# Kernel optimization log

Measured on AMD Instinct MI355X. Metric: run time of the kernel, lower is better.

Reference implementation:

```python
import jax, jax.numpy as jnp
import numpy as np
from jax import lax

B, H, W = 16, 1024, 1024


def _bayer_masks(h, w, pattern='RGGB'):
    ch = {c: np.zeros((h, w), dtype=bool) for c in 'RGB'}
    for c, (y, x) in zip(pattern.upper(), [(0, 0), (0, 1), (1, 0), (1, 1)]):
        ch[c][y::2, x::2] = True
    return ch['R'], ch['G'], ch['B']


def _kernels():
    GR_GB = np.asarray([[0, 0, -1, 0, 0], [0, 0, 2, 0, 0], [-1, 2, 4, 2, -1],
                        [0, 0, 2, 0, 0], [0, 0, -1, 0, 0]], dtype=np.float64) / 8
    Rg_RB_Bg_BR = np.asarray([[0, 0, 0.5, 0, 0], [0, -1, 0, -1, 0], [-1, 4, 5, 4, -1],
                              [0, -1, 0, -1, 0], [0, 0, 0.5, 0, 0]], dtype=np.float64) / 8
    Rg_BR_Bg_RB = Rg_RB_Bg_BR.T
    Rb_BB_Br_RR = np.asarray([[0, 0, -1.5, 0, 0], [0, 2, 0, 2, 0], [-1.5, 0, 6, 0, -1.5],
                              [0, 2, 0, 2, 0], [0, 0, -1.5, 0, 0]], dtype=np.float64) / 8
    # torch code stores rot90(k=2) copies and feeds them to F.conv2d (cross-correlation)
    rot = lambda k: np.ascontiguousarray(np.rot90(k, 2)).astype(np.float32)
    return rot(GR_GB), rot(Rg_RB_Bg_BR), rot(Rg_BR_Bg_RB), rot(Rb_BB_Br_RR)


def setup_inputs() -> dict:
    key = jax.random.key(0)
    cfa = jax.random.uniform(key, (B, 1, H, W), dtype=jnp.float32)
    k1, k2, k3, k4 = _kernels()
    return {
        'CFA_inputs': cfa,
        'GR_GB': jnp.asarray(k1),
        'Rg_RB_Bg_BR': jnp.asarray(k2),
        'Rg_BR_Bg_RB': jnp.asarray(k3),
        'Rb_BB_Br_RR': jnp.asarray(k4),
    }


def _conv5(x, k):  # x: [B,1,H,W], k: [5,5]; cross-correlation, padding=2
    return lax.conv_general_dilated(
        x, k[None, None].astype(x.dtype), (1, 1), ((2, 2), (2, 2)),
        dimension_numbers=('NCHW', 'OIHW', 'NCHW'))


def reference(CFA_inputs, GR_GB, Rg_RB_Bg_BR, Rg_BR_Bg_RB, Rb_BB_Br_RR):
    h, w = CFA_inputs.shape[2], CFA_inputs.shape[3]
    R_m, G_m, B_m = _bayer_masks(h, w, 'RGGB')

    # static row/column selector masks (numpy, concrete at trace time)
    R_r = np.any(R_m, axis=1)[:, None] & np.ones((h, w), dtype=bool)
    R_c = np.any(R_m, axis=0)[None, :] & np.ones((h, w), dtype=bool)
    B_r = np.any(B_m, axis=1)[:, None] & np.ones((h, w), dtype=bool)
    B_c = np.any(B_m, axis=0)[None, :] & np.ones((h, w), dtype=bool)

    m = lambda a: jnp.asarray(a[None, None])  # -> [1,1,H,W] bool

    R = CFA_inputs * m(R_m).astype(CFA_inputs.dtype)
    G = CFA_inputs * m(G_m).astype(CFA_inputs.dtype)
    Bp = CFA_inputs * m(B_m).astype(CFA_inputs.dtype)

    GR_GB_res = _conv5(CFA_inputs, GR_GB)
    RBg_RBBR = _conv5(CFA_inputs, Rg_RB_Bg_BR)
    RBg_BRRB = _conv5(CFA_inputs, Rg_BR_Bg_RB)
    RBgr_BBRR = _conv5(CFA_inputs, Rb_BB_Br_RR)

    G = jnp.where(m(R_m | B_m), GR_GB_res, G)

    Rr_Bc = m(R_r & B_c)
    Br_Rc = m(B_r & R_c)
    Br_Bc = m(B_r & B_c)
    Rr_Rc = m(R_r & R_c)

    R = jnp.where(Rr_Bc, RBg_RBBR, R)
    R = jnp.where(Br_Rc, RBg_BRRB, R)
    Bp = jnp.where(Br_Rc, RBg_RBBR, Bp)
    Bp = jnp.where(Rr_Bc, RBg_BRRB, Bp)
    R = jnp.where(Br_Bc, RBgr_BBRR, R)
    Bp = jnp.where(Rr_Rc, RBgr_BBRR, Bp)

    return jnp.concatenate([R, G, Bp], axis=1)  # [B,3,H,W]
```

## Files before the change

### kernel.cpp

```cpp
#include <hip/hip_runtime.h>


constexpr int Bn = 16, Hn = 1024, Wn = 1024;
constexpr int RS = 16;

typedef float vfloat4 __attribute__((ext_vector_type(4)));

__global__ __launch_bounds__(256) void demosaic_v3(
    const float* __restrict__ src, float* __restrict__ out)
{
    const int t  = threadIdx.x;
    const int y0 = blockIdx.x * RS;
    const int b  = blockIdx.y;

    const float* sb = sb = src + (size_t)b * Hn * Wn;

    const bool tL = (t == 0);
    const bool tR = (t == 255);
    const int xl = tL ? 0 : (4 * t - 4);
    const int xr = tR ? (Wn - 4) : (4 * t + 4);

    float row[5][8];

    auto loadrow = [&](int gy, float* r) {
        const bool valid = ((unsigned)gy < (unsigned)Hn);
        const int gyc = valid ? gy : 0;
        const float* p = sb + (size_t)gyc * Wn;
        const vfloat4 c  = *(const vfloat4*)(p + 4 * t);
        const vfloat4 lq = *(const vfloat4*)(p + xl);
        const vfloat4 rq = *(const vfloat4*)(p + xr);
        r[0] = tL ? 0.f : lq.z;
        r[1] = tL ? 0.f : lq.w;
        r[2] = c.x; r[3] = c.y; r[4] = c.z; r[5] = c.w;
        r[6] = tR ? 0.f : rq.x;
        r[7] = tR ? 0.f : rq.y;
        if (!valid) {
            #pragma unroll
            for (int k = 0; k < 8; ++k) r[k] = 0.f;
        }
    };

    #pragma unroll
    for (int i = 0; i < 4; ++i) loadrow(y0 - 2 + i, row[i]);

    const size_t HW = (size_t)Hn * Wn;
    float* ob = out + (size_t)b * 3 * HW + (size_t)y0 * Wn + 4 * t;

    #pragma unroll
    for (int i = 0; i < RS; ++i) {
        loadrow(y0 + i + 2, row[(i + 4) % 5]);

        const float* r0 = row[(i + 0) % 5];
        const float* r1 = row[(i + 1) % 5];
        const float* r2 = row[(i + 2) % 5];
        const float* r3 = row[(i + 3) % 5];
        const float* r4 = row[(i + 4) % 5];

        float R[4], G[4], Bc[4];
        #pragma unroll
        for (int j = 0; j < 4; ++j) {
            const float c   = r2[j + 2];
            const float h1  = r2[j + 1] + r2[j + 3];
            const float v1  = r1[j + 2] + r3[j + 2];
            const float h2  = r2[j] + r2[j + 4];
            const float v2s = r0[j + 2] + r4[j + 2];
            const float ax2 = h2 + v2s;
            const float dg  = r1[j + 1] + r1[j + 3] + r3[j + 1] + r3[j + 3];

            const int py = i & 1;
            const int px = j & 1;
            if (px == 0 && py == 0) {
                R[j] = c;
                G[j] = 0.5f * c + 0.25f * (h1 + v1) - 0.125f * ax2;
                Bc[j] = 0.75f * c + 0.25f * dg - 0.1875f * ax2;
            } else if (px == 1 && py == 0) {
                R[j] = 0.625f * c + 0.5f * h1 - 0.125f * h2 + 0.0625f * v2s - 0.125f * dg;
                G[j] = c;
                Bc[j] = 0.625f * c + 0.5f * v1 - 0.125f * v2s + 0.0625f * h2 - 0.125f * dg;
            } else if (px == 0 && py == 1) {
                R[j] = 0.625f * c + 0.5f * v1 - 0.125f * v2s + 0.0625f * h2 - 0.125f * dg;
                G[j] = c;
                Bc[j] = 0.625f * c + 0.5f * h1 - 0.125f * h2 + 0.0625f * v2s - 0.125f * dg;
            } else {
                R[j] = 0.75f * c + 0.25f * dg - 0.1875f * ax2;
                G[j] = 0.5f * c + 0.25f * (h1 + v1) - 0.125f * ax2;
                Bc[j] = c;
            }
        }

        vfloat4 r4v = {R[0], R[1], R[2], R[3]};
        vfloat4 g4v = {G[0], G[1], G[2], G[3]};
        vfloat4 b4v = {Bc[0], Bc[1], Bc[2], Bc[3]};
        float* o = ob + (size_t)i * Wn;
        __builtin_nontemporal_store(r4v, (vfloat4*)o);
        __builtin_nontemporal_store(g4v, (vfloat4*)(o + HW));
        __builtin_nontemporal_store(b4v, (vfloat4*)(o + 2 * HW));
    }
}

extern "C" void kernel_launch(void* const* d_in, const int* in_sizes, int n_in,
                              void* d_out, int out_size, void* d_ws, size_t ws_size,
                              hipStream_t stream) {
    const float* cfa = (const float*)d_in[0];
    float* out = (float*)d_out;

    dim3 grid(Hn / RS, Bn);
    demosaic_v3<<<grid, dim3(256), 0, stream>>>(cfa, out);
}
```

Measured before the change: 259.4 us.

## Use 4-row tiles with all halo rows loaded upfront instead of rolling window

Each block now handles 4 output rows instead of 16 and loads all 8 needed input rows (center plus left/right quads) at the start rather than streaming one row per iteration. This raises memory-level parallelism and quadruples the number of blocks. The cost is more redundant halo reads, about 2x input re-reading instead of 1.25x, and more registers per thread.

Result: no change. 254.6 us (-1.9%).

```diff
diff --git a/kernel.cpp b/kernel.cpp
--- a/kernel.cpp
+++ b/kernel.cpp
@@ -2,59 +2,61 @@
 
 
 constexpr int Bn = 16, Hn = 1024, Wn = 1024;
-constexpr int RS = 16;
+constexpr int TR = 4;
 
 typedef float vfloat4 __attribute__((ext_vector_type(4)));
 
-__global__ __launch_bounds__(256) void demosaic_v3(
+__global__ __launch_bounds__(256) void demosaic_v4(
     const float* __restrict__ src, float* __restrict__ out)
 {
     const int t  = threadIdx.x;
-    const int y0 = blockIdx.x * RS;
+    const int y0 = blockIdx.x * TR;
     const int b  = blockIdx.y;
 
-    const float* sb = sb = src + (size_t)b * Hn * Wn;
+    const float* sb = src + (size_t)b * Hn * Wn;
 
     const bool tL = (t == 0);
     const bool tR = (t == 255);
-    const int xl = tL ? 0 : (4 * t - 4);
-    const int xr = tR ? (Wn - 4) : (4 * t + 4);
+    const int xc = 4 * t;
+    const int xl = tL ? 0 : xc - 4;
+    const int xr = tR ? (Wn - 4) : (xc + 4);
 
-    float row[5][8];
+    vfloat4 Lq[8], Cq[8], Rq[8];
+    #pragma unroll
+    for (int r = 0; r < 8; ++r) {
+        int gy = y0 - 2 + r;
+        int gyc = gy < 0 ? 0 : (gy > Hn - 1 ? Hn - 1 : gy);
+        const float* p = sb + (size_t)gyc * Wn;
+        Cq[r] = *(const vfloat4*)(p + xc);
+        Lq[r] = *(const vfloat4*)(p + xl);
+        Rq[r] = *(const vfloat4*)(p + xr);
+    }
 
-    auto loadrow = [&](int gy, float* r) {
-        const bool valid = ((unsigned)gy < (unsigned)Hn);
-        const int gyc = valid ? gy : 0;
-        const float* p = sb + (size_t)gyc * Wn;
-        const vfloat4 c  = *(const vfloat4*)(p + 4 * t);
-        const vfloat4 lq = *(const vfloat4*)(p + xl);
-        const vfloat4 rq = *(const vfloat4*)(p + xr);
-        r[0] = tL ? 0.f : lq.z;
-        r[1] = tL ? 0.f : lq.w;
-        r[2] = c.x; r[3] = c.y; r[4] = c.z; r[5] = c.w;
-        r[6] = tR ? 0.f : rq.x;
-        r[7] = tR ? 0.f : rq.y;
-        if (!valid) {
-            #pragma unroll
-            for (int k = 0; k < 8; ++k) r[k] = 0.f;
-        }
-    };
+    float v[8][8];
+    #pragma unroll
+    for (int r = 0; r < 8; ++r) {
+        int gy = y0 - 2 + r;
+        const bool val = ((unsigned)gy < (unsigned)Hn);
+        v[r][0] = (val && !tL) ? Lq[r].z : 0.f;
+        v[r][1] = (val && !tL) ? Lq[r].w : 0.f;
+        v[r][2] = val ? Cq[r].x : 0.f;
+        v[r][3] = val ? Cq[r].y : 0.f;
+        v[r][4] = val ? Cq[r].z : 0.f;
+        v[r][5] = val ? Cq[r].w : 0.f;
+        v[r][6] = (val && !tR) ? Rq[r].x : 0.f;
+        v[r][7] = (val && !tR) ? Rq[r].y : 0.f;
+    }
+
+    const size_t HW = (size_t)Hn * Wn;
+    float* ob = out + (size_t)b * 3 * HW + (size_t)y0 * Wn + xc;
 
     #pragma unroll
-    for (int i = 0; i < 4; ++i) loadrow(y0 - 2 + i, row[i]);
-
-    const size_t HW = (size_t)Hn * Wn;
-    float* ob = out + (size_t)b * 3 * HW + (size_t)y0 * Wn + 4 * t;
-
-    #pragma unroll
-    for (int i = 0; i < RS; ++i) {
-        loadrow(y0 + i + 2, row[(i + 4) % 5]);
-
-        const float* r0 = row[(i + 0) % 5];
-        const float* r1 = row[(i + 1) % 5];
-        const float* r2 = row[(i + 2) % 5];
-        const float* r3 = row[(i + 3) % 5];
-        const float* r4 = row[(i + 4) % 5];
+    for (int i = 0; i < TR; ++i) {
+        const float* r0 = v[i + 0];
+        const float* r1 = v[i + 1];
+        const float* r2 = v[i + 2];
+        const float* r3 = v[i + 3];
+        const float* r4 = v[i + 4];
 
         float R[4], G[4], Bc[4];
         #pragma unroll
@@ -104,6 +106,6 @@
     const float* cfa = (const float*)d_in[0];
     float* out = (float*)d_out;
 
-    dim3 grid(Hn / RS, Bn);
-    demosaic_v3<<<grid, dim3(256), 0, stream>>>(cfa, out);
+    dim3 grid(Hn / TR, Bn);
+    demosaic_v4<<<grid, dim3(256), 0, stream>>>(cfa, out);
 }
```
